# Kernel optimization log

Measured on AMD Instinct MI355X. Metric: run time of the kernel, lower is better.

The kernel has to match this reference:

```python
import jax, jax.numpy as jnp
import numpy as np

N_CODES = 4096
D = 256


def setup_inputs() -> dict:
    key = jax.random.key(0)
    k_v, k_w = jax.random.split(key)
    v = jax.random.normal(k_v, (8, 2048, D), dtype=jnp.float32)
    # Embedding init ~ N(0,1), then softmax over dim=1, then row 0 set to 1/d (empty feature)
    w = jax.random.normal(k_w, (N_CODES, D), dtype=jnp.float32)
    w = jax.nn.softmax(w, axis=1)
    w = w.at[0].set(1.0 / D)
    return {"v": v, "vectors": w}


def reference(v, vectors):
    n, d = vectors.shape
    cb = vectors[1:]  # exclude the fixed empty feature at index 0
    # ||v - c||^2 = ||v||^2 - 2 v.c + ||c||^2  (avoids [..., n, d] intermediate)
    v2 = jnp.sum(v * v, axis=-1, keepdims=True)              # [..., 1]
    c2 = jnp.sum(cb * cb, axis=-1)                           # [n-1]
    diff = v2 - 2.0 * jnp.einsum('...d,nd->...n', v, cb) + c2  # [..., n-1]
    idx = jnp.argmin(diff, axis=-1) + 1                      # [...]
    # empty-feature mask: any component differs from 1/d
    mask = jnp.any(v != (1.0 / d), axis=-1)
    idx = jnp.where(mask, idx, 0)
    out = vectors[idx]                                       # gather == onehot @ vectors
    loss = jnp.mean(jnp.square(out - jax.lax.stop_gradient(v)))
    used = jnp.array(0, dtype=jnp.int32)  # eval mode: usage pool is empty
    return out, idx, loss, used
```

## Files before the change

kernel.cpp:

```cpp
#include <hip/hip_runtime.h>
#include <hip/hip_fp16.h>
#include <math.h>
#include <stdint.h>


#define M_TOTAL 16384
#define NCODES  4096
#define D_DIM   256

#define OUT_OFF_IDX  (M_TOTAL * D_DIM)
#define OUT_OFF_LOSS (OUT_OFF_IDX + M_TOTAL)

#define NPART 16
#define VPLANE (M_TOTAL * D_DIM)

typedef _Float16 half8 __attribute__((ext_vector_type(8)));
typedef _Float16 half4v __attribute__((ext_vector_type(4)));
typedef float    float16v __attribute__((ext_vector_type(16)));

__global__ __launch_bounds__(64) void prep_v_kernel(
    const float* __restrict__ X, _Float16* __restrict__ hi, _Float16* __restrict__ lo,
    float* __restrict__ sq)
{
  __shared__ float T[64 * 66];
  const int l = threadIdx.x;
  const int r0 = blockIdx.x * 64;
  float rj[8];
  float s0 = 0.0f, s1 = 0.0f;
#pragma unroll
  for (int kt = 0; kt < 4; ++kt) {
    __syncthreads();
#pragma unroll
    for (int s = 0; s < 16; ++s) {
      const int row = s * 4 + (l >> 4), c4 = l & 15;
      const size_t go = (size_t)(r0 + row) * D_DIM + kt * 64 + c4 * 4;
      float4 v = *(const float4*)(X + go);
      float xs[4] = {v.x, v.y, v.z, v.w};
      union { half4v h; _Float16 e[4]; } uh, ul;
#pragma unroll
      for (int j = 0; j < 4; ++j) {
        float sc = xs[j] * 1024.0f;
        _Float16 h = (_Float16)sc;
        uh.e[j] = h;
        ul.e[j] = (_Float16)(sc - (float)h);
      }
      *(half4v*)(hi + go) = uh.h;
      *(half4v*)(lo + go) = ul.h;
      *(float4*)&T[row * 66 + c4 * 4] = v;
    }
    __syncthreads();
#pragma unroll
    for (int c4 = 0; c4 < 16; ++c4) {
      float4 v = *(const float4*)&T[l * 66 + c4 * 4];
      float e[4] = {v.x, v.y, v.z, v.w};
#pragma unroll
      for (int t = 0; t < 4; ++t) {
        const int k = kt * 64 + c4 * 4 + t;
        const int j = k & 7;
        float sqv = __fmul_rn(e[t], e[t]);
        if ((k & 127) < 8) rj[j] = sqv;
        else rj[j] = __fadd_rn(rj[j], sqv);
      }
    }
    if (kt == 1) s0 = __fadd_rn(__fadd_rn(__fadd_rn(rj[0], rj[1]), __fadd_rn(rj[2], rj[3])),
                                __fadd_rn(__fadd_rn(rj[4], rj[5]), __fadd_rn(rj[6], rj[7])));
    if (kt == 3) s1 = __fadd_rn(__fadd_rn(__fadd_rn(rj[0], rj[1]), __fadd_rn(rj[2], rj[3])),
                                __fadd_rn(__fadd_rn(rj[4], rj[5]), __fadd_rn(rj[6], rj[7])));
  }
  sq[r0 + l] = __fadd_rn(s0, s1);
}

__global__ __launch_bounds__(64) void prep_w_kernel(
    const float* __restrict__ W, _Float16* __restrict__ Bp, float* __restrict__ c2)
{
  __shared__ float T[64 * 66];
  const int l = threadIdx.x;
  const int r0 = blockIdx.x * 64;
  const int panel = (r0 >> 5) + (l >> 5);
  const int nin = l & 31;
  float rj[8];
  float s0 = 0.0f, s1 = 0.0f;
#pragma unroll
  for (int kt = 0; kt < 4; ++kt) {
    __syncthreads();
#pragma unroll
    for (int s = 0; s < 16; ++s) {
      const int row = s * 4 + (l >> 4), c4 = l & 15;
      *(float4*)&T[row * 66 + c4 * 4] =
          *(const float4*)(W + (size_t)(r0 + row) * D_DIM + kt * 64 + c4 * 4);
    }
    __syncthreads();
    union { half8 v; _Float16 e[8]; } uh, ul;
#pragma unroll
    for (int c4 = 0; c4 < 16; ++c4) {
      float4 v = *(const float4*)&T[l * 66 + c4 * 4];
      float e[4] = {v.x, v.y, v.z, v.w};
#pragma unroll
      for (int t = 0; t < 4; ++t) {
        const int k = kt * 64 + c4 * 4 + t;
        float sc = e[t] * 1024.0f;
        _Float16 h = (_Float16)sc;
        uh.e[(c4 & 1) * 4 + t] = h;
        ul.e[(c4 & 1) * 4 + t] = (_Float16)(sc - (float)h);
        const int j = k & 7;
        float sqv = __fmul_rn(e[t], e[t]);
        if ((k & 127) < 8) rj[j] = sqv;
        else rj[j] = __fadd_rn(rj[j], sqv);
      }
      if (c4 & 1) {
        const int g = kt * 8 + (c4 >> 1);
        const int kstep = g >> 1, lhi = g & 1;
        _Float16* dst = Bp + ((size_t)panel * 16 + kstep) * 2048 + lhi * 256 + nin * 8;
        *(half8*)dst = uh.v;
        *(half8*)(dst + 1024) = ul.v;
      }
    }
    if (kt == 1) s0 = __fadd_rn(__fadd_rn(__fadd_rn(rj[0], rj[1]), __fadd_rn(rj[2], rj[3])),
                                __fadd_rn(__fadd_rn(rj[4], rj[5]), __fadd_rn(rj[6], rj[7])));
    if (kt == 3) s1 = __fadd_rn(__fadd_rn(__fadd_rn(rj[0], rj[1]), __fadd_rn(rj[2], rj[3])),
                                __fadd_rn(__fadd_rn(rj[4], rj[5]), __fadd_rn(rj[6], rj[7])));
  }
  c2[r0 + l] = __fadd_rn(s0, s1);
}

__global__ __launch_bounds__(256, 1) void vq_mfma_kernel(
    const _Float16* __restrict__ Vhi, const _Float16* __restrict__ Vlo,
    const _Float16* __restrict__ Bp,
    const float* __restrict__ v2, const float* __restrict__ c2,
    uint64_t* __restrict__ pk)
{
  __shared__ __align__(16) _Float16 smem[16384];
  __shared__ uint64_t red2[512];

  const int tid  = threadIdx.x;
  const int lane = tid & 63;
  const int wave = tid >> 6;
  const int wr = wave >> 1, wc = wave & 1;
  const int l31 = lane & 31, lhi = lane >> 5;

  const int bid = blockIdx.x;
  const int panel = (bid & 7) * 2 + ((bid >> 3) & 1);
  const int mblk  = bid >> 4;
  const int m0 = mblk * 256;
  const int n0 = panel * 256;
  const int p32 = (n0 >> 5) + wc * 4;

  int src[4], dst[4];
#pragma unroll
  for (int u = 0; u < 4; ++u) {
    const int g = tid + 256 * u, m = g >> 2, kb = g & 3;
    src[u] = (m0 + m) * D_DIM + kb * 8;
    dst[u] = m * 32 + (kb ^ (m & 3)) * 8;
  }

  float16v acc[4][4];
#pragma unroll
  for (int mb = 0; mb < 4; ++mb)
#pragma unroll
    for (int nb = 0; nb < 4; ++nb) acc[mb][nb] = (float16v)0.0f;

  half8 sh[4], sl[4];
#pragma unroll
  for (int u = 0; u < 4; ++u) {
    sh[u] = *(const half8*)(Vhi + src[u]);
    sl[u] = *(const half8*)(Vlo + src[u]);
  }

  half8 bh[2][4], bl[2][4];
#pragma unroll
  for (int nb = 0; nb < 4; ++nb) {
    const _Float16* bp = Bp + ((size_t)(p32 + nb) * 16 + 0) * 2048 + lane * 8;
    bh[0][nb] = *(const half8*)bp;
    bl[0][nb] = *(const half8*)(bp + 1024);
  }

#pragma unroll
  for (int kt = 0; kt < 8; ++kt) {
    if (kt) __syncthreads();
#pragma unroll
    for (int u = 0; u < 4; ++u) {
      *(half8*)(smem + dst[u])        = sh[u];
      *(half8*)(smem + 8192 + dst[u]) = sl[u];
    }
    __syncthreads();
    if (kt < 7) {
#pragma unroll
      for (int u = 0; u < 4; ++u) {
        sh[u] = *(const half8*)(Vhi + src[u] + (kt + 1) * 32);
        sl[u] = *(const half8*)(Vlo + src[u] + (kt + 1) * 32);
      }
    }
#pragma unroll
    for (int ks = 0; ks < 2; ++ks) {
      const int kstep = kt * 2 + ks;
      const int cur = kstep & 1, nxt = cur ^ 1;
      if (kstep < 15) {
#pragma unroll
        for (int nb = 0; nb < 4; ++nb) {
          const _Float16* bp = Bp + ((size_t)(p32 + nb) * 16 + kstep + 1) * 2048 + lane * 8;
          bh[nxt][nb] = *(const half8*)bp;
          bl[nxt][nb] = *(const half8*)(bp + 1024);
        }
      }
      half8 ah[4], al[4];
#pragma unroll
      for (int mb = 0; mb < 4; ++mb) {
        const int m = wr * 128 + mb * 32 + l31;
        const int c = (ks * 2 + lhi) ^ (m & 3);
        ah[mb] = *(const half8*)(smem + m * 32 + c * 8);
        al[mb] = *(const half8*)(smem + 8192 + m * 32 + c * 8);
      }
#pragma unroll
      for (int nb = 0; nb < 4; ++nb)
#pragma unroll
        for (int mb = 0; mb < 4; ++mb)
          acc[mb][nb] = __builtin_amdgcn_mfma_f32_32x32x16_f16(ah[mb], bh[cur][nb], acc[mb][nb], 0, 0, 0);
#pragma unroll
      for (int nb = 0; nb < 4; ++nb)
#pragma unroll
        for (int mb = 0; mb < 4; ++mb)
          acc[mb][nb] = __builtin_amdgcn_mfma_f32_32x32x16_f16(ah[mb], bl[cur][nb], acc[mb][nb], 0, 0, 0);
#pragma unroll
      for (int nb = 0; nb < 4; ++nb)
#pragma unroll
        for (int mb = 0; mb < 4; ++mb)
          acc[mb][nb] = __builtin_amdgcn_mfma_f32_32x32x16_f16(al[mb], bh[cur][nb], acc[mb][nb], 0, 0, 0);
    }
  }

  float c2r[4];
#pragma unroll
  for (int nb = 0; nb < 4; ++nb) c2r[nb] = c2[n0 + wc * 128 + nb * 32 + l31];

  __syncthreads();
  uint64_t* wbuf = (uint64_t*)smem + wave * 1024;

#pragma unroll
  for (int mb = 0; mb < 4; ++mb) {
#pragma unroll
    for (int r = 0; r < 16; ++r) {
      const int mrow = wr * 128 + mb * 32 + (r & 3) + 8 * (r >> 2) + 4 * lhi;
      const float v2m = v2[m0 + mrow];
      uint64_t b = ~0ULL;
#pragma unroll
      for (int nb = 0; nb < 4; ++nb) {
        const int n = n0 + wc * 128 + nb * 32 + l31;
        float dot = acc[mb][nb][r] * 0x1p-20f;
        float dd  = __fadd_rn(__fsub_rn(v2m, 2.0f * dot), c2r[nb]);
        if (n == 0) dd = INFINITY;
        uint64_t p = ((uint64_t)__float_as_uint(dd) << 32) | (uint32_t)n;
        if (p < b) b = p;
      }
      wbuf[r * 64 + lhi * 32 + l31] = b;
    }
    __syncthreads();
    {
      const int f = lane >> 1, hf = lane & 1;
      const uint64_t* rp = wbuf + f * 32 + hf * 16;
      uint64_t m = rp[0];
#pragma unroll
      for (int i = 1; i < 16; ++i) { uint64_t v = rp[i]; if (v < m) m = v; }
      uint64_t o = __shfl_xor((unsigned long long)m, 1);
      if (o < m) m = o;
      if (hf == 0) {
        const int r_ = f >> 1, lh2 = f & 1;
        const int mrow = wr * 128 + mb * 32 + (r_ & 3) + 8 * (r_ >> 2) + 4 * lh2;
        red2[mrow * 2 + wc] = m;
      }
    }
    __syncthreads();
  }

  uint64_t a0 = red2[tid * 2], a1 = red2[tid * 2 + 1];
  pk[(size_t)panel * M_TOTAL + m0 + tid] = a0 < a1 ? a0 : a1;
}

__global__ __launch_bounds__(256) void gather_kernel(
    const float* __restrict__ V, const float* __restrict__ W,
    const uint64_t* __restrict__ pk,
    float* __restrict__ out, float* __restrict__ outIdx,
    float* __restrict__ lossPartial)
{
  const int q = blockIdx.x * 4 + (threadIdx.x >> 6);
  const int l = threadIdx.x & 63;
  uint64_t b = (l < NPART) ? pk[(size_t)l * M_TOTAL + q] : ~0ULL;
#pragma unroll
  for (int off = 32; off; off >>= 1) {
    uint64_t o = __shfl_xor((unsigned long long)b, off);
    if (o < b) b = o;
  }
  float4 vv = *(const float4*)(V + (size_t)q * D_DIM + l * 4);
  const float inv = 0.00390625f;
  bool ne = (vv.x != inv) | (vv.y != inv) | (vv.z != inv) | (vv.w != inv);
  const int idx = __ballot(ne) ? (int)(uint32_t)b : 0;
  float4 o4 = *(const float4*)(W + (size_t)idx * D_DIM + l * 4);
  *(float4*)(out + (size_t)q * D_DIM + l * 4) = o4;
  if (l == 0) outIdx[q] = (float)idx;
  float dx = o4.x - vv.x, dy = o4.y - vv.y, dz = o4.z - vv.z, dw = o4.w - vv.w;
  float s = dx * dx + dy * dy + dz * dz + dw * dw;
#pragma unroll
  for (int off = 32; off; off >>= 1) s += __shfl_xor(s, off);
  if (l == 0) lossPartial[q] = s;
}

__global__ __launch_bounds__(256) void finalize_kernel(
    const float* __restrict__ lossPartial, float* __restrict__ out)
{
  const int t = threadIdx.x;
  __shared__ float red[256];
  float s = 0.0f;
  for (int i = t; i < M_TOTAL; i += 256) s += lossPartial[i];
  red[t] = s;
  __syncthreads();
  for (int st = 128; st > 0; st >>= 1) {
    if (t < st) red[t] += red[t + st];
    __syncthreads();
  }
  if (t == 0) {
    out[0] = (float)((double)red[0] / (double)(M_TOTAL * D_DIM));
    out[1] = 0.0f;
  }
}

extern "C" void kernel_launch(void* const* d_in, const int* in_sizes, int n_in,
                              void* d_out, int out_size, void* d_ws, size_t ws_size,
                              hipStream_t stream) {
  const float* V = (const float*)d_in[0];
  const float* W = (const float*)d_in[1];
  float* out = (float*)d_out;

  _Float16* Vhi = (_Float16*)d_out;
  _Float16* Vlo = Vhi + VPLANE;

  char* ws = (char*)d_ws;
  _Float16* Bp  = (_Float16*)(ws);
  float*    c2  = (float*)(ws + 8388608);
  float*    v2  = (float*)(ws + 8388608 + 16384);
  uint64_t* pk  = (uint64_t*)(ws + 8388608 + 16384 + 65536);
  float* lossPartial = (float*)(ws + 8388608 + 16384 + 65536 + 2097152);

  prep_w_kernel<<<NCODES / 64, 64, 0, stream>>>(W, Bp, c2);
  prep_v_kernel<<<M_TOTAL / 64, 64, 0, stream>>>(V, Vhi, Vlo, v2);
  vq_mfma_kernel<<<1024, 256, 0, stream>>>(Vhi, Vlo, Bp, v2, c2, pk);
  gather_kernel<<<M_TOTAL / 4, 256, 0, stream>>>(V, W, pk, out, out + OUT_OFF_IDX, lossPartial);
  finalize_kernel<<<1, 256, 0, stream>>>(lossPartial, out + OUT_OFF_LOSS);
}
```

Before: 223.4 us.

## Halve MFMA N-tile for two blocks per CU and widen prep kernels

The distance GEMM block now covers 256x128 instead of 256x256, halving the accumulator registers, doubling the grid to 2048 blocks and the partial-argmin planes to 32, and requesting two blocks per CU via launch bounds. The reduction scratch is padded to a stride of 33 to avoid LDS bank conflicts. The prep kernels are rewritten to use 256 threads per 16 rows, with a direct per-thread fp16 hi/lo split and a shuffle-based squared-norm reduction. The extra blocks re-read the V tiles twice as often and the gather must merge twice as many partials.

```diff
diff --git a/kernel.cpp b/kernel.cpp
--- a/kernel.cpp
+++ b/kernel.cpp
@@ -11,126 +11,109 @@
 #define OUT_OFF_IDX  (M_TOTAL * D_DIM)
 #define OUT_OFF_LOSS (OUT_OFF_IDX + M_TOTAL)
 
-#define NPART 16
+#define NPART 32
 #define VPLANE (M_TOTAL * D_DIM)
 
 typedef _Float16 half8 __attribute__((ext_vector_type(8)));
-typedef _Float16 half4v __attribute__((ext_vector_type(4)));
 typedef float    float16v __attribute__((ext_vector_type(16)));
 
-__global__ __launch_bounds__(64) void prep_v_kernel(
+__global__ __launch_bounds__(256) void prep_v_kernel(
     const float* __restrict__ X, _Float16* __restrict__ hi, _Float16* __restrict__ lo,
     float* __restrict__ sq)
 {
-  __shared__ float T[64 * 66];
-  const int l = threadIdx.x;
-  const int r0 = blockIdx.x * 64;
-  float rj[8];
-  float s0 = 0.0f, s1 = 0.0f;
-#pragma unroll
-  for (int kt = 0; kt < 4; ++kt) {
-    __syncthreads();
-#pragma unroll
-    for (int s = 0; s < 16; ++s) {
-      const int row = s * 4 + (l >> 4), c4 = l & 15;
-      const size_t go = (size_t)(r0 + row) * D_DIM + kt * 64 + c4 * 4;
-      float4 v = *(const float4*)(X + go);
-      float xs[4] = {v.x, v.y, v.z, v.w};
-      union { half4v h; _Float16 e[4]; } uh, ul;
-#pragma unroll
-      for (int j = 0; j < 4; ++j) {
-        float sc = xs[j] * 1024.0f;
-        _Float16 h = (_Float16)sc;
-        uh.e[j] = h;
-        ul.e[j] = (_Float16)(sc - (float)h);
-      }
-      *(half4v*)(hi + go) = uh.h;
-      *(half4v*)(lo + go) = ul.h;
-      *(float4*)&T[row * 66 + c4 * 4] = v;
-    }
-    __syncthreads();
-#pragma unroll
-    for (int c4 = 0; c4 < 16; ++c4) {
-      float4 v = *(const float4*)&T[l * 66 + c4 * 4];
-      float e[4] = {v.x, v.y, v.z, v.w};
-#pragma unroll
-      for (int t = 0; t < 4; ++t) {
-        const int k = kt * 64 + c4 * 4 + t;
-        const int j = k & 7;
-        float sqv = __fmul_rn(e[t], e[t]);
-        if ((k & 127) < 8) rj[j] = sqv;
-        else rj[j] = __fadd_rn(rj[j], sqv);
-      }
-    }
-    if (kt == 1) s0 = __fadd_rn(__fadd_rn(__fadd_rn(rj[0], rj[1]), __fadd_rn(rj[2], rj[3])),
-                                __fadd_rn(__fadd_rn(rj[4], rj[5]), __fadd_rn(rj[6], rj[7])));
-    if (kt == 3) s1 = __fadd_rn(__fadd_rn(__fadd_rn(rj[0], rj[1]), __fadd_rn(rj[2], rj[3])),
-                                __fadd_rn(__fadd_rn(rj[4], rj[5]), __fadd_rn(rj[6], rj[7])));
-  }
-  sq[r0 + l] = __fadd_rn(s0, s1);
-}
-
-__global__ __launch_bounds__(64) void prep_w_kernel(
+  __shared__ float T[16 * 264];
+  const int t = threadIdx.x;
+  const int rloc = t >> 4, seg = t & 15;
+  const int row = blockIdx.x * 16 + rloc;
+  const float* src = X + (size_t)row * D_DIM + seg * 16;
+  float4 x[4];
+#pragma unroll
+  for (int u = 0; u < 4; ++u) x[u] = ((const float4*)src)[u];
+  union { half8 v; _Float16 e[8]; } uh[2], ul[2];
+#pragma unroll
+  for (int u = 0; u < 4; ++u) {
+    float e4[4] = {x[u].x, x[u].y, x[u].z, x[u].w};
+#pragma unroll
+    for (int j = 0; j < 4; ++j) {
+      const int e = u * 4 + j;
+      float s = e4[j] * 1024.0f;
+      _Float16 h = (_Float16)s;
+      uh[e >> 3].e[e & 7] = h;
+      ul[e >> 3].e[e & 7] = (_Float16)(s - (float)h);
+    }
+    *(float4*)&T[rloc * 264 + seg * 16 + u * 4] = x[u];
+  }
+  _Float16* hd = hi + (size_t)row * D_DIM + seg * 16;
+  _Float16* ld = lo + (size_t)row * D_DIM + seg * 16;
+  *(half8*)hd = uh[0].v; *(half8*)(hd + 8) = uh[1].v;
+  *(half8*)ld = ul[0].v; *(half8*)(ld + 8) = ul[1].v;
+  __syncthreads();
+  const int half = (t >> 3) & 1, j = t & 7;
+  const float* tr = &T[rloc * 264 + half * 128 + j];
+  float r = __fmul_rn(tr[0], tr[0]);
+#pragma unroll
+  for (int i = 1; i < 16; ++i) { float e = tr[8 * i]; r = __fadd_rn(r, __fmul_rn(e, e)); }
+  r = __fadd_rn(r, __shfl_xor(r, 1));
+  r = __fadd_rn(r, __shfl_xor(r, 2));
+  r = __fadd_rn(r, __shfl_xor(r, 4));
+  r = __fadd_rn(r, __shfl_xor(r, 8));
+  if ((t & 15) == 0) sq[row] = r;
+}
+
+__global__ __launch_bounds__(256) void prep_w_kernel(
     const float* __restrict__ W, _Float16* __restrict__ Bp, float* __restrict__ c2)
 {
-  __shared__ float T[64 * 66];
-  const int l = threadIdx.x;
-  const int r0 = blockIdx.x * 64;
-  const int panel = (r0 >> 5) + (l >> 5);
-  const int nin = l & 31;
-  float rj[8];
-  float s0 = 0.0f, s1 = 0.0f;
-#pragma unroll
-  for (int kt = 0; kt < 4; ++kt) {
-    __syncthreads();
-#pragma unroll
-    for (int s = 0; s < 16; ++s) {
-      const int row = s * 4 + (l >> 4), c4 = l & 15;
-      *(float4*)&T[row * 66 + c4 * 4] =
-          *(const float4*)(W + (size_t)(r0 + row) * D_DIM + kt * 64 + c4 * 4);
-    }
-    __syncthreads();
-    union { half8 v; _Float16 e[8]; } uh, ul;
-#pragma unroll
-    for (int c4 = 0; c4 < 16; ++c4) {
-      float4 v = *(const float4*)&T[l * 66 + c4 * 4];
-      float e[4] = {v.x, v.y, v.z, v.w};
-#pragma unroll
-      for (int t = 0; t < 4; ++t) {
-        const int k = kt * 64 + c4 * 4 + t;
-        float sc = e[t] * 1024.0f;
-        _Float16 h = (_Float16)sc;
-        uh.e[(c4 & 1) * 4 + t] = h;
-        ul.e[(c4 & 1) * 4 + t] = (_Float16)(sc - (float)h);
-        const int j = k & 7;
-        float sqv = __fmul_rn(e[t], e[t]);
-        if ((k & 127) < 8) rj[j] = sqv;
-        else rj[j] = __fadd_rn(rj[j], sqv);
-      }
-      if (c4 & 1) {
-        const int g = kt * 8 + (c4 >> 1);
-        const int kstep = g >> 1, lhi = g & 1;
-        _Float16* dst = Bp + ((size_t)panel * 16 + kstep) * 2048 + lhi * 256 + nin * 8;
-        *(half8*)dst = uh.v;
-        *(half8*)(dst + 1024) = ul.v;
-      }
-    }
-    if (kt == 1) s0 = __fadd_rn(__fadd_rn(__fadd_rn(rj[0], rj[1]), __fadd_rn(rj[2], rj[3])),
-                                __fadd_rn(__fadd_rn(rj[4], rj[5]), __fadd_rn(rj[6], rj[7])));
-    if (kt == 3) s1 = __fadd_rn(__fadd_rn(__fadd_rn(rj[0], rj[1]), __fadd_rn(rj[2], rj[3])),
-                                __fadd_rn(__fadd_rn(rj[4], rj[5]), __fadd_rn(rj[6], rj[7])));
-  }
-  c2[r0 + l] = __fadd_rn(s0, s1);
-}
-
-__global__ __launch_bounds__(256, 1) void vq_mfma_kernel(
+  __shared__ float T[16 * 264];
+  const int t = threadIdx.x;
+  const int rloc = t >> 4, seg = t & 15;
+  const int row = blockIdx.x * 16 + rloc;
+  const float* src = W + (size_t)row * D_DIM + seg * 16;
+  float4 x[4];
+#pragma unroll
+  for (int u = 0; u < 4; ++u) x[u] = ((const float4*)src)[u];
+  union { half8 v; _Float16 e[8]; } uh[2], ul[2];
+#pragma unroll
+  for (int u = 0; u < 4; ++u) {
+    float e4[4] = {x[u].x, x[u].y, x[u].z, x[u].w};
+#pragma unroll
+    for (int j = 0; j < 4; ++j) {
+      const int e = u * 4 + j;
+      float s = e4[j] * 1024.0f;
+      _Float16 h = (_Float16)s;
+      uh[e >> 3].e[e & 7] = h;
+      ul[e >> 3].e[e & 7] = (_Float16)(s - (float)h);
+    }
+    *(float4*)&T[rloc * 264 + seg * 16 + u * 4] = x[u];
+  }
+  const int panel = row >> 5, nin = row & 31;
+  _Float16* dst = Bp + ((size_t)panel * 16 + seg) * 2048 + nin * 8;
+#pragma unroll
+  for (int lh = 0; lh < 2; ++lh) {
+    *(half8*)(dst + lh * 256)        = uh[lh].v;
+    *(half8*)(dst + 1024 + lh * 256) = ul[lh].v;
+  }
+  __syncthreads();
+  const int half = (t >> 3) & 1, j = t & 7;
+  const float* tr = &T[rloc * 264 + half * 128 + j];
+  float r = __fmul_rn(tr[0], tr[0]);
+#pragma unroll
+  for (int i = 1; i < 16; ++i) { float e = tr[8 * i]; r = __fadd_rn(r, __fmul_rn(e, e)); }
+  r = __fadd_rn(r, __shfl_xor(r, 1));
+  r = __fadd_rn(r, __shfl_xor(r, 2));
+  r = __fadd_rn(r, __shfl_xor(r, 4));
+  r = __fadd_rn(r, __shfl_xor(r, 8));
+  if ((t & 15) == 0) c2[row] = r;
+}
+
+__global__ __launch_bounds__(256, 2) void vq_mfma_kernel(
     const _Float16* __restrict__ Vhi, const _Float16* __restrict__ Vlo,
     const _Float16* __restrict__ Bp,
     const float* __restrict__ v2, const float* __restrict__ c2,
     uint64_t* __restrict__ pk)
 {
-  __shared__ __align__(16) _Float16 smem[16384];
-  __shared__ uint64_t red2[512];
+  __shared__ __align__(16) char smem_raw[37888];
+  _Float16* As = (_Float16*)smem_raw;
+  uint64_t* red2 = (uint64_t*)(smem_raw + 33792);
 
   const int tid  = threadIdx.x;
   const int lane = tid & 63;
@@ -139,11 +122,11 @@
   const int l31 = lane & 31, lhi = lane >> 5;
 
   const int bid = blockIdx.x;
-  const int panel = (bid & 7) * 2 + ((bid >> 3) & 1);
-  const int mblk  = bid >> 4;
+  const int panel = (bid & 7) * 4 + ((bid >> 3) & 3);
+  const int mblk  = bid >> 5;
   const int m0 = mblk * 256;
-  const int n0 = panel * 256;
-  const int p32 = (n0 >> 5) + wc * 4;
+  const int n0 = panel * 128;
+  const int p32 = panel * 4 + wc * 2;
 
   int src[4], dst[4];
 #pragma unroll
@@ -153,11 +136,11 @@
     dst[u] = m * 32 + (kb ^ (m & 3)) * 8;
   }
 
-  float16v acc[4][4];
+  float16v acc[4][2];
 #pragma unroll
   for (int mb = 0; mb < 4; ++mb)
 #pragma unroll
-    for (int nb = 0; nb < 4; ++nb) acc[mb][nb] = (float16v)0.0f;
+    for (int nb = 0; nb < 2; ++nb) acc[mb][nb] = (float16v)0.0f;
 
   half8 sh[4], sl[4];
 #pragma unroll
@@ -166,21 +149,20 @@
     sl[u] = *(const half8*)(Vlo + src[u]);
   }
 
-  half8 bh[2][4], bl[2][4];
-#pragma unroll
-  for (int nb = 0; nb < 4; ++nb) {
-    const _Float16* bp = Bp + ((size_t)(p32 + nb) * 16 + 0) * 2048 + lane * 8;
+  half8 bh[2][2], bl[2][2];
+#pragma unroll
+  for (int nb = 0; nb < 2; ++nb) {
+    const _Float16* bp = Bp + ((size_t)(p32 + nb) * 16) * 2048 + lane * 8;
     bh[0][nb] = *(const half8*)bp;
     bl[0][nb] = *(const half8*)(bp + 1024);
   }
 
-#pragma unroll
   for (int kt = 0; kt < 8; ++kt) {
     if (kt) __syncthreads();
 #pragma unroll
     for (int u = 0; u < 4; ++u) {
-      *(half8*)(smem + dst[u])        = sh[u];
-      *(half8*)(smem + 8192 + dst[u]) = sl[u];
+      *(half8*)(As + dst[u])        = sh[u];
+      *(half8*)(As + 8192 + dst[u]) = sl[u];
     }
     __syncthreads();
     if (kt < 7) {
@@ -196,7 +178,7 @@
       const int cur = kstep & 1, nxt = cur ^ 1;
       if (kstep < 15) {
 #pragma unroll
-        for (int nb = 0; nb < 4; ++nb) {
+        for (int nb = 0; nb < 2; ++nb) {
           const _Float16* bp = Bp + ((size_t)(p32 + nb) * 16 + kstep + 1) * 2048 + lane * 8;
           bh[nxt][nb] = *(const half8*)bp;
           bl[nxt][nb] = *(const half8*)(bp + 1024);
@@ -207,56 +189,56 @@
       for (int mb = 0; mb < 4; ++mb) {
         const int m = wr * 128 + mb * 32 + l31;
         const int c = (ks * 2 + lhi) ^ (m & 3);
-        ah[mb] = *(const half8*)(smem + m * 32 + c * 8);
-        al[mb] = *(const half8*)(smem + 8192 + m * 32 + c * 8);
-      }
-#pragma unroll
-      for (int nb = 0; nb < 4; ++nb)
+        ah[mb] = *(const half8*)(As + m * 32 + c * 8);
+        al[mb] = *(const half8*)(As + 8192 + m * 32 + c * 8);
+      }
+#pragma unroll
+      for (int nb = 0; nb < 2; ++nb)
 #pragma unroll
         for (int mb = 0; mb < 4; ++mb)
           acc[mb][nb] = __builtin_amdgcn_mfma_f32_32x32x16_f16(ah[mb], bh[cur][nb], acc[mb][nb], 0, 0, 0);
 #pragma unroll
-      for (int nb = 0; nb < 4; ++nb)
+      for (int nb = 0; nb < 2; ++nb)
 #pragma unroll
         for (int mb = 0; mb < 4; ++mb)
           acc[mb][nb] = __builtin_amdgcn_mfma_f32_32x32x16_f16(ah[mb], bl[cur][nb], acc[mb][nb], 0, 0, 0);
 #pragma unroll
-      for (int nb = 0; nb < 4; ++nb)
+      for (int nb = 0; nb < 2; ++nb)
 #pragma unroll
         for (int mb = 0; mb < 4; ++mb)
           acc[mb][nb] = __builtin_amdgcn_mfma_f32_32x32x16_f16(al[mb], bh[cur][nb], acc[mb][nb], 0, 0, 0);
     }
   }
 
-  float c2r[4];
-#pragma unroll
-  for (int nb = 0; nb < 4; ++nb) c2r[nb] = c2[n0 + wc * 128 + nb * 32 + l31];
+  float c2r[2];
+#pragma unroll
+  for (int nb = 0; nb < 2; ++nb) c2r[nb] = c2[n0 + wc * 64 + nb * 32 + l31];
 
   __syncthreads();
-  uint64_t* wbuf = (uint64_t*)smem + wave * 1024;
+  uint64_t* wbuf = (uint64_t*)smem_raw + wave * 1056;
 
 #pragma unroll
   for (int mb = 0; mb < 4; ++mb) {
 #pragma unroll
     for (int r = 0; r < 16; ++r) {
-      const int mrow = wr * 128 + mb * 32 + (r & 3) + 8 * (r >> 2) + 4 * lhi;
-      const float v2m = v2[m0 + mrow];
+      const int rowin = (r & 3) + 8 * (r >> 2) + 4 * lhi;
+      const float v2m = v2[m0 + wr * 128 + mb * 32 + rowin];
       uint64_t b = ~0ULL;
 #pragma unroll
-      for (int nb = 0; nb < 4; ++nb) {
-        const int n = n0 + wc * 128 + nb * 32 + l31;
+      for (int nb = 0; nb < 2; ++nb) {
+        const int n = n0 + wc * 64 + nb * 32 + l31;
         float dot = acc[mb][nb][r] * 0x1p-20f;
         float dd  = __fadd_rn(__fsub_rn(v2m, 2.0f * dot), c2r[nb]);
         if (n == 0) dd = INFINITY;
         uint64_t p = ((uint64_t)__float_as_uint(dd) << 32) | (uint32_t)n;
         if (p < b) b = p;
       }
-      wbuf[r * 64 + lhi * 32 + l31] = b;
+      wbuf[(r * 2 + lhi) * 33 + l31] = b;
     }
     __syncthreads();
     {
       const int f = lane >> 1, hf = lane & 1;
-      const uint64_t* rp = wbuf + f * 32 + hf * 16;
+      const uint64_t* rp = wbuf + f * 33 + hf * 16;
       uint64_t m = rp[0];
 #pragma unroll
       for (int i = 1; i < 16; ++i) { uint64_t v = rp[i]; if (v < m) m = v; }
@@ -264,8 +246,8 @@
       if (o < m) m = o;
       if (hf == 0) {
         const int r_ = f >> 1, lh2 = f & 1;
-        const int mrow = wr * 128 + mb * 32 + (r_ & 3) + 8 * (r_ >> 2) + 4 * lh2;
-        red2[mrow * 2 + wc] = m;
+        const int rowin = (r_ & 3) + 8 * (r_ >> 2) + 4 * lh2;
+        red2[(wr * 128 + mb * 32 + rowin) * 2 + wc] = m;
       }
     }
     __syncthreads();
@@ -337,11 +319,11 @@
   float*    c2  = (float*)(ws + 8388608);
   float*    v2  = (float*)(ws + 8388608 + 16384);
   uint64_t* pk  = (uint64_t*)(ws + 8388608 + 16384 + 65536);
-  float* lossPartial = (float*)(ws + 8388608 + 16384 + 65536 + 2097152);
-
-  prep_w_kernel<<<NCODES / 64, 64, 0, stream>>>(W, Bp, c2);
-  prep_v_kernel<<<M_TOTAL / 64, 64, 0, stream>>>(V, Vhi, Vlo, v2);
-  vq_mfma_kernel<<<1024, 256, 0, stream>>>(Vhi, Vlo, Bp, v2, c2, pk);
+  float* lossPartial = (float*)(ws + 8388608 + 16384 + 65536 + 4194304);
+
+  prep_w_kernel<<<NCODES / 16, 256, 0, stream>>>(W, Bp, c2);
+  prep_v_kernel<<<M_TOTAL / 16, 256, 0, stream>>>(V, Vhi, Vlo, v2);
+  vq_mfma_kernel<<<2048, 256, 0, stream>>>(Vhi, Vlo, Bp, v2, c2, pk);
   gather_kernel<<<M_TOTAL / 4, 256, 0, stream>>>(V, W, pk, out, out + OUT_OFF_IDX, lossPartial);
   finalize_kernel<<<1, 256, 0, stream>>>(lossPartial, out + OUT_OFF_LOSS);
 }
```

Measured after the change: 212.8 us. 4.8% less time.
